# Performance work log

Measured on AMD Instinct MI355X. Metric: run time of the kernel, lower is better.

Reference implementation:

```python
import jax, jax.numpy as jnp
import numpy as np

B, I, O, C = 8192, 256, 256, 32


def setup_inputs() -> dict:
    key = jax.random.key(0)
    k1, k2, k3, k4 = jax.random.split(key, 4)
    x = jax.random.normal(k1, (B, I), dtype=jnp.float32)
    idx_channel = jax.random.randint(k2, (B,), 0, C, dtype=jnp.int64)
    # learned params per init_kwargs: weight [O, I, C], bias [O, C]
    weight = jax.random.normal(k3, (O, I, C), dtype=jnp.float32) * (1.0 / np.sqrt(I))
    bias = jax.random.normal(k4, (O, C), dtype=jnp.float32) * (1.0 / np.sqrt(O))
    return {"x": x, "idx_channel": idx_channel, "weight": weight, "bias": bias}


def reference(x, idx_channel, weight, bias):
    # Original: one_hot(idx) @ weight then batched matvec; mathematically this is
    # a per-sample gather of weight[..., idx[b]] followed by a batched GEMV + bias.
    w_sel = jnp.take(weight, idx_channel, axis=2)          # [O, I, B]
    b_sel = jnp.take(bias, idx_channel, axis=1).T          # [B, O]
    out = jnp.einsum('oib,bi->bo', w_sel, x) + b_sel       # [B, O]
    return out
```

## Files before the change

### kernel.cpp

```cpp
#include <hip/hip_runtime.h>
#include <hip/hip_bf16.h>

#define NB 8192
#define NI 256
#define NO 256
#define NC 32

typedef __attribute__((ext_vector_type(8))) short short8;
typedef __attribute__((ext_vector_type(4))) float floatx4;

#define WS_COUNTS_OFF 0
#define WS_LISTS_OFF  (4u << 10)
#define WS_XB_OFF     (1u << 20)
#define WS_WT_OFF     (5u << 20)

static __device__ __forceinline__ unsigned short f2bf(float f) {
    __hip_bfloat16 h = __float2bfloat16(f);
    return *(unsigned short*)&h;
}

__global__ void k_bucket(const int* __restrict__ idx,
                         unsigned int* __restrict__ counts,
                         unsigned short* __restrict__ lists) {
    int b = blockIdx.x * 256 + threadIdx.x;
    int c = idx[b] & (NC - 1);
    unsigned int slot = atomicAdd(&counts[c], 1u);
    lists[c * NB + slot] = (unsigned short)b;
}

__global__ void k_convert_x(const float* __restrict__ x,
                            unsigned short* __restrict__ xb) {
    size_t t = (size_t)blockIdx.x * 256 + threadIdx.x;
    const float4* src = (const float4*)(x + t * 8);
    float4 a = src[0], b = src[1];
    unsigned short r[8];
    r[0] = f2bf(a.x); r[1] = f2bf(a.y); r[2] = f2bf(a.z); r[3] = f2bf(a.w);
    r[4] = f2bf(b.x); r[5] = f2bf(b.y); r[6] = f2bf(b.z); r[7] = f2bf(b.w);
    *(uint4*)(xb + t * 8) = *(uint4*)r;
}

__global__ void k_transpose(const float* __restrict__ w,
                            unsigned short* __restrict__ wT) {
    int g = blockIdx.x * 256 + threadIdx.x;
    const float4* src = (const float4*)(w + (size_t)g * NC);
    unsigned short vals[NC];
#pragma unroll
    for (int s = 0; s < 8; ++s) {
        float4 v = src[s];
        vals[s * 4 + 0] = f2bf(v.x);
        vals[s * 4 + 1] = f2bf(v.y);
        vals[s * 4 + 2] = f2bf(v.z);
        vals[s * 4 + 3] = f2bf(v.w);
    }
#pragma unroll
    for (int c = 0; c < NC; ++c) {
        wT[(size_t)c * (NO * NI) + g] = vals[c];
    }
}

__launch_bounds__(256)
__global__ void k_gemm(const unsigned short* __restrict__ xb,
                       const unsigned short* __restrict__ wT,
                       const float* __restrict__ bias,
                       const unsigned int* __restrict__ counts,
                       const unsigned short* __restrict__ lists,
                       float* __restrict__ out) {
    const int c  = blockIdx.x;
    const int o0 = blockIdx.y * 64;
    const int cnt = (int)counts[c];
    const int m0 = blockIdx.z * 64;
    if (m0 >= cnt) return;

    __shared__ unsigned short As[64][136];
    __shared__ unsigned short Bs[64][136];
    __shared__ int blist[64];

    const int tid = threadIdx.x;
    if (tid < 64) {
        int mr = m0 + tid;
        blist[tid] = (int)lists[c * NB + (mr < cnt ? mr : m0)];
    }
    __syncthreads();

    const int wv   = tid >> 6;
    const int lane = tid & 63;
    const int lrc  = lane & 15;
    const int koff = (lane >> 4) * 8;

    floatx4 acc[4];
#pragma unroll
    for (int ms = 0; ms < 4; ++ms) acc[ms] = (floatx4){0.f, 0.f, 0.f, 0.f};

    const unsigned short* wTc = wT + ((size_t)c * NO + o0) * NI;

#pragma unroll
    for (int kt = 0; kt < 2; ++kt) {
        const int kb = kt * 128;
#pragma unroll
        for (int s = 0; s < 4; ++s) {
            int lin = tid + s * 256;
            int row = lin >> 4;
            int c8  = (lin & 15) * 8;
            *(uint4*)&As[row][c8] = *(const uint4*)(xb + (size_t)blist[row] * NI + kb + c8);
            *(uint4*)&Bs[row][c8] = *(const uint4*)(wTc + (size_t)row * NI + kb + c8);
        }
        __syncthreads();

        const int n0 = wv * 16;
#pragma unroll
        for (int k0 = 0; k0 < 4; ++k0) {
            short8 bfrag = *(const short8*)&Bs[n0 + lrc][k0 * 32 + koff];
#pragma unroll
            for (int ms = 0; ms < 4; ++ms) {
                short8 afrag = *(const short8*)&As[ms * 16 + lrc][k0 * 32 + koff];
                acc[ms] = __builtin_amdgcn_mfma_f32_16x16x32_bf16(afrag, bfrag, acc[ms], 0, 0, 0);
            }
        }
        __syncthreads();
    }

    const int o = o0 + wv * 16 + lrc;
    const float bv = bias[o * NC + c];
    const int rbase = (lane >> 4) * 4;
#pragma unroll
    for (int ms = 0; ms < 4; ++ms) {
#pragma unroll
        for (int r = 0; r < 4; ++r) {
            int row = ms * 16 + rbase + r;
            if (m0 + row < cnt) {
                out[(size_t)blist[row] * NO + o] = acc[ms][r] + bv;
            }
        }
    }
}

extern "C" void kernel_launch(void* const* d_in, const int* in_sizes, int n_in,
                              void* d_out, int out_size, void* d_ws, size_t ws_size,
                              hipStream_t stream) {
    const float* x    = (const float*)d_in[0];
    const int*   idx  = (const int*)d_in[1];
    const float* w    = (const float*)d_in[2];
    const float* bias = (const float*)d_in[3];
    float* out = (float*)d_out;

    char* ws = (char*)d_ws;
    unsigned int*   counts = (unsigned int*)(ws + WS_COUNTS_OFF);
    unsigned short* lists  = (unsigned short*)(ws + WS_LISTS_OFF);
    unsigned short* xb     = (unsigned short*)(ws + WS_XB_OFF);
    unsigned short* wT     = (unsigned short*)(ws + WS_WT_OFF);

    hipMemsetAsync(counts, 0, NC * sizeof(unsigned int), stream);
    k_bucket<<<NB / 256, 256, 0, stream>>>(idx, counts, lists);
    k_convert_x<<<(NB * NI / 8) / 256, 256, 0, stream>>>(x, xb);
    k_transpose<<<(NO * NI) / 256, 256, 0, stream>>>(w, wT);
    dim3 grid(NC, NO / 64, NB / 64);
    k_gemm<<<grid, 256, 0, stream>>>(xb, wT, bias, counts, lists, out);
}
```

Baseline: 98.55 us.

## Fuse bucketing, x conversion and weight transpose into one prep kernel; shrink GEMM grid

The memset and the three preprocessing kernels (bucketing, x to bf16, weight transpose to bf16) are merged into one launch that picks its role from the block index. Bucketing now gives each channel one block that scans all indices and uses a shared-memory atomic counter, so the separate memset of the counts is no longer needed. The GEMM grid's z dimension drops from 128 to 8, and each block loops over m-tiles with a stride of 8, so far fewer blocks launch only to exit early. This cuts launch and dispatch overhead. In exchange, the bucketing blocks each read the whole index array redundantly, and the per-channel list order is no longer deterministic.

```diff
diff --git a/kernel.cpp b/kernel.cpp
--- a/kernel.cpp
+++ b/kernel.cpp
@@ -19,42 +19,61 @@
     return *(unsigned short*)&h;
 }
 
-__global__ void k_bucket(const int* __restrict__ idx,
-                         unsigned int* __restrict__ counts,
-                         unsigned short* __restrict__ lists) {
-    int b = blockIdx.x * 256 + threadIdx.x;
-    int c = idx[b] & (NC - 1);
-    unsigned int slot = atomicAdd(&counts[c], 1u);
-    lists[c * NB + slot] = (unsigned short)b;
-}
+#define PREP_CONV0 32
+#define PREP_TRAN0 (32 + 1024)
+#define PREP_BLOCKS (PREP_TRAN0 + 256)
 
-__global__ void k_convert_x(const float* __restrict__ x,
-                            unsigned short* __restrict__ xb) {
-    size_t t = (size_t)blockIdx.x * 256 + threadIdx.x;
-    const float4* src = (const float4*)(x + t * 8);
-    float4 a = src[0], b = src[1];
-    unsigned short r[8];
-    r[0] = f2bf(a.x); r[1] = f2bf(a.y); r[2] = f2bf(a.z); r[3] = f2bf(a.w);
-    r[4] = f2bf(b.x); r[5] = f2bf(b.y); r[6] = f2bf(b.z); r[7] = f2bf(b.w);
-    *(uint4*)(xb + t * 8) = *(uint4*)r;
-}
+__global__ __launch_bounds__(256) void k_prep(
+        const int* __restrict__ idx,
+        const float* __restrict__ x,
+        const float* __restrict__ w,
+        unsigned int* __restrict__ counts,
+        unsigned short* __restrict__ lists,
+        unsigned short* __restrict__ xb,
+        unsigned short* __restrict__ wT) {
+    const int bid = blockIdx.x;
+    const int tid = threadIdx.x;
 
-__global__ void k_transpose(const float* __restrict__ w,
-                            unsigned short* __restrict__ wT) {
-    int g = blockIdx.x * 256 + threadIdx.x;
-    const float4* src = (const float4*)(w + (size_t)g * NC);
-    unsigned short vals[NC];
+    if (bid < PREP_CONV0) {
+        __shared__ unsigned int lcnt;
+        if (tid == 0) lcnt = 0u;
+        __syncthreads();
+        const int c = bid;
+        const int4* idx4 = (const int4*)idx;
+        for (int t = tid; t < NB / 4; t += 256) {
+            int4 v = idx4[t];
+            int b0 = t * 4;
+            if (v.x == c) lists[c * NB + atomicAdd(&lcnt, 1u)] = (unsigned short)(b0 + 0);
+            if (v.y == c) lists[c * NB + atomicAdd(&lcnt, 1u)] = (unsigned short)(b0 + 1);
+            if (v.z == c) lists[c * NB + atomicAdd(&lcnt, 1u)] = (unsigned short)(b0 + 2);
+            if (v.w == c) lists[c * NB + atomicAdd(&lcnt, 1u)] = (unsigned short)(b0 + 3);
+        }
+        __syncthreads();
+        if (tid == 0) counts[c] = lcnt;
+    } else if (bid < PREP_TRAN0) {
+        size_t t = (size_t)(bid - PREP_CONV0) * 256 + tid;
+        const float4* src = (const float4*)(x + t * 8);
+        float4 a = src[0], b = src[1];
+        unsigned short r[8];
+        r[0] = f2bf(a.x); r[1] = f2bf(a.y); r[2] = f2bf(a.z); r[3] = f2bf(a.w);
+        r[4] = f2bf(b.x); r[5] = f2bf(b.y); r[6] = f2bf(b.z); r[7] = f2bf(b.w);
+        *(uint4*)(xb + t * 8) = *(uint4*)r;
+    } else {
+        int g = (bid - PREP_TRAN0) * 256 + tid;
+        const float4* src = (const float4*)(w + (size_t)g * NC);
+        unsigned short vals[NC];
 #pragma unroll
-    for (int s = 0; s < 8; ++s) {
-        float4 v = src[s];
-        vals[s * 4 + 0] = f2bf(v.x);
-        vals[s * 4 + 1] = f2bf(v.y);
-        vals[s * 4 + 2] = f2bf(v.z);
-        vals[s * 4 + 3] = f2bf(v.w);
-    }
+        for (int s = 0; s < 8; ++s) {
+            float4 v = src[s];
+            vals[s * 4 + 0] = f2bf(v.x);
+            vals[s * 4 + 1] = f2bf(v.y);
+            vals[s * 4 + 2] = f2bf(v.z);
+            vals[s * 4 + 3] = f2bf(v.w);
+        }
 #pragma unroll
-    for (int c = 0; c < NC; ++c) {
-        wT[(size_t)c * (NO * NI) + g] = vals[c];
+        for (int c = 0; c < NC; ++c) {
+            wT[(size_t)c * (NO * NI) + g] = vals[c];
+        }
     }
 }
 
@@ -68,69 +87,71 @@
     const int c  = blockIdx.x;
     const int o0 = blockIdx.y * 64;
     const int cnt = (int)counts[c];
-    const int m0 = blockIdx.z * 64;
-    if (m0 >= cnt) return;
 
     __shared__ unsigned short As[64][136];
     __shared__ unsigned short Bs[64][136];
     __shared__ int blist[64];
 
-    const int tid = threadIdx.x;
-    if (tid < 64) {
-        int mr = m0 + tid;
-        blist[tid] = (int)lists[c * NB + (mr < cnt ? mr : m0)];
-    }
-    __syncthreads();
-
+    const int tid  = threadIdx.x;
     const int wv   = tid >> 6;
     const int lane = tid & 63;
     const int lrc  = lane & 15;
     const int koff = (lane >> 4) * 8;
-
-    floatx4 acc[4];
-#pragma unroll
-    for (int ms = 0; ms < 4; ++ms) acc[ms] = (floatx4){0.f, 0.f, 0.f, 0.f};
+    const int rbase = (lane >> 4) * 4;
 
     const unsigned short* wTc = wT + ((size_t)c * NO + o0) * NI;
+    const int o = o0 + wv * 16 + lrc;
+    const float bv = bias[o * NC + c];
 
-#pragma unroll
-    for (int kt = 0; kt < 2; ++kt) {
-        const int kb = kt * 128;
-#pragma unroll
-        for (int s = 0; s < 4; ++s) {
-            int lin = tid + s * 256;
-            int row = lin >> 4;
-            int c8  = (lin & 15) * 8;
-            *(uint4*)&As[row][c8] = *(const uint4*)(xb + (size_t)blist[row] * NI + kb + c8);
-            *(uint4*)&Bs[row][c8] = *(const uint4*)(wTc + (size_t)row * NI + kb + c8);
+    for (int mt = blockIdx.z; mt * 64 < cnt; mt += 8) {
+        const int m0 = mt * 64;
+        if (tid < 64) {
+            int mr = m0 + tid;
+            blist[tid] = (int)lists[c * NB + (mr < cnt ? mr : m0)];
         }
         __syncthreads();
 
-        const int n0 = wv * 16;
+        floatx4 acc[4];
 #pragma unroll
-        for (int k0 = 0; k0 < 4; ++k0) {
-            short8 bfrag = *(const short8*)&Bs[n0 + lrc][k0 * 32 + koff];
+        for (int ms = 0; ms < 4; ++ms) acc[ms] = (floatx4){0.f, 0.f, 0.f, 0.f};
+
 #pragma unroll
-            for (int ms = 0; ms < 4; ++ms) {
-                short8 afrag = *(const short8*)&As[ms * 16 + lrc][k0 * 32 + koff];
-                acc[ms] = __builtin_amdgcn_mfma_f32_16x16x32_bf16(afrag, bfrag, acc[ms], 0, 0, 0);
+        for (int kt = 0; kt < 2; ++kt) {
+            const int kb = kt * 128;
+#pragma unroll
+            for (int s = 0; s < 4; ++s) {
+                int lin = tid + s * 256;
+                int row = lin >> 4;
+                int c8  = (lin & 15) * 8;
+                *(uint4*)&As[row][c8] = *(const uint4*)(xb + (size_t)blist[row] * NI + kb + c8);
+                *(uint4*)&Bs[row][c8] = *(const uint4*)(wTc + (size_t)row * NI + kb + c8);
+            }
+            __syncthreads();
+
+            const int n0 = wv * 16;
+#pragma unroll
+            for (int k0 = 0; k0 < 4; ++k0) {
+                short8 bfrag = *(const short8*)&Bs[n0 + lrc][k0 * 32 + koff];
+#pragma unroll
+                for (int ms = 0; ms < 4; ++ms) {
+                    short8 afrag = *(const short8*)&As[ms * 16 + lrc][k0 * 32 + koff];
+                    acc[ms] = __builtin_amdgcn_mfma_f32_16x16x32_bf16(afrag, bfrag, acc[ms], 0, 0, 0);
+                }
+            }
+            __syncthreads();
+        }
+
+#pragma unroll
+        for (int ms = 0; ms < 4; ++ms) {
+#pragma unroll
+            for (int r = 0; r < 4; ++r) {
+                int row = ms * 16 + rbase + r;
+                if (m0 + row < cnt) {
+                    out[(size_t)blist[row] * NO + o] = acc[ms][r] + bv;
+                }
             }
         }
         __syncthreads();
-    }
-
-    const int o = o0 + wv * 16 + lrc;
-    const float bv = bias[o * NC + c];
-    const int rbase = (lane >> 4) * 4;
-#pragma unroll
-    for (int ms = 0; ms < 4; ++ms) {
-#pragma unroll
-        for (int r = 0; r < 4; ++r) {
-            int row = ms * 16 + rbase + r;
-            if (m0 + row < cnt) {
-                out[(size_t)blist[row] * NO + o] = acc[ms][r] + bv;
-            }
-        }
     }
 }
 
@@ -149,10 +170,7 @@
     unsigned short* xb     = (unsigned short*)(ws + WS_XB_OFF);
     unsigned short* wT     = (unsigned short*)(ws + WS_WT_OFF);
 
-    hipMemsetAsync(counts, 0, NC * sizeof(unsigned int), stream);
-    k_bucket<<<NB / 256, 256, 0, stream>>>(idx, counts, lists);
-    k_convert_x<<<(NB * NI / 8) / 256, 256, 0, stream>>>(x, xb);
-    k_transpose<<<(NO * NI) / 256, 256, 0, stream>>>(w, wT);
-    dim3 grid(NC, NO / 64, NB / 64);
+    k_prep<<<PREP_BLOCKS, 256, 0, stream>>>(idx, x, w, counts, lists, xb, wT);
+    dim3 grid(NC, NO / 64, 8);
     k_gemm<<<grid, 256, 0, stream>>>(xb, wT, bias, counts, lists, out);
 }
```

New measurement: 82.97 us. -15.8%, faster.
